# Optimization experiments

Hardware: AMD Instinct MI355X
Metric: run time of the kernel (lower is better)

## Reference

```python
import jax, jax.numpy as jnp
import numpy as np

N, E, G = 51200, 819200, 256            # nodes, directed edges, graphs
N2, A, E2 = 102400, 204800, 409600      # 2-sets, assignments, 2-set edges
D, L, NI2, NAF = 64, 5, 36, 40          # emb_dim, num_layer, num_i_2, num_atom_features
EPS = 1e-5


def _seg_sum(v, seg, n):
    return jax.ops.segment_sum(v, seg, num_segments=n)


def _seg_mean(v, seg, n):
    s = jax.ops.segment_sum(v, seg, num_segments=n)
    c = jax.ops.segment_sum(jnp.ones((v.shape[0],), v.dtype), seg, num_segments=n)
    return s / jnp.maximum(c, 1.0)[:, None]


def setup_inputs() -> dict:
    key = jax.random.key(0)
    ks = iter(jax.random.split(key, 64))
    nrm = lambda shape: jax.random.normal(next(ks), shape, jnp.float32) * 0.1
    x = jax.random.normal(next(ks), (N, NAF), jnp.float32)
    edge_index = jax.random.randint(next(ks), (2, E), 0, N, dtype=jnp.int32)
    edge_attr = jnp.stack([jax.random.randint(next(ks), (E,), 0, 4, dtype=jnp.int32),
                           jax.random.randint(next(ks), (E,), 0, 3, dtype=jnp.int32)], axis=1)
    batch = jnp.repeat(jnp.arange(G, dtype=jnp.int32), N // G)
    iso_type_2 = jax.nn.one_hot(jax.random.randint(next(ks), (N2,), 0, NI2), NI2, dtype=jnp.float32)
    edge_index_2 = jax.random.randint(next(ks), (2, E2), 0, N2, dtype=jnp.int32)
    assignment_index_2 = jnp.stack([jax.random.randint(next(ks), (A,), 0, N, dtype=jnp.int32),
                                    jnp.repeat(jnp.arange(N2, dtype=jnp.int32), 2)], axis=0)
    batch_2 = jnp.repeat(jnp.arange(G, dtype=jnp.int32), N2 // G)
    params = dict(
        emb_W=nrm((NAF, D)), emb_b=jnp.zeros((D,), jnp.float32),
        gin_W1=nrm((L, D, 2 * D)), gin_b1=jnp.zeros((L, 2 * D), jnp.float32),
        gin_W2=nrm((L, 2 * D, D)), gin_b2=jnp.zeros((L, D), jnp.float32),
        eemb1=nrm((L, 6, D)), eemb2=nrm((L, 3, D)),
        bn_gamma=jnp.ones((L, D), jnp.float32), bn_beta=jnp.zeros((L, D), jnp.float32),
        iso1_rel_W=nrm((D + NI2, D)), iso1_rel_b=jnp.zeros((D,), jnp.float32),
        iso1_root_W=nrm((D + NI2, D)),
        iso2_rel_W=nrm((D, D)), iso2_rel_b=jnp.zeros((D,), jnp.float32),
        iso2_root_W=nrm((D, D)),
        ro_W0=nrm((2 * D, D)), ro_b0=jnp.zeros((D,), jnp.float32),
        ro_W1=nrm((D, D // 2)), ro_b1=jnp.zeros((D // 2,), jnp.float32),
        ro_W2=nrm((D // 2, D // 4)), ro_b2=jnp.zeros((D // 4,), jnp.float32),
        last_W=nrm((D // 4, 1)), last_b=jnp.zeros((1,), jnp.float32),
    )
    return dict(x=x, edge_index=edge_index, edge_attr=edge_attr, batch=batch,
                iso_type_2=iso_type_2, edge_index_2=edge_index_2,
                assignment_index_2=assignment_index_2, batch_2=batch_2, **params)


def _forward(x, iso_type_2, emb_W, emb_b, gin_W1, gin_b1, gin_W2, gin_b2,
             eemb1, eemb2, bn_gamma, bn_beta,
             iso1_rel_W, iso1_rel_b, iso1_root_W, iso2_rel_W, iso2_rel_b, iso2_root_W,
             ro_W0, ro_b0, ro_W1, ro_b1, ro_W2, ro_b2, last_W, last_b,
             edge_index, edge_attr, batch, edge_index_2, assignment_index_2, batch_2):
    # --- GIN stack with edge-feature embeddings and self loops ---
    loop = jnp.arange(N, dtype=edge_index.dtype)
    src = jnp.concatenate([edge_index[0], loop])
    dst = jnp.concatenate([edge_index[1], loop])
    sl_attr = jnp.tile(jnp.array([[4, 0]], dtype=edge_attr.dtype), (N, 1))
    ea = jnp.concatenate([edge_attr, sl_attr], axis=0)  # [E+N, 2]

    h = jax.nn.relu(x @ emb_W + emb_b)  # x_embedding1
    for l in range(L):
        e = eemb1[l][ea[:, 0]] + eemb2[l][ea[:, 1]]      # [E+N, D]
        agg = _seg_sum(h[src] + e, dst, N)               # gather + scatter-add
        h2 = jax.nn.relu(agg @ gin_W1[l] + gin_b1[l]) @ gin_W2[l] + gin_b2[l]
        mu = jnp.mean(h2, axis=0)
        var = jnp.var(h2, axis=0)                        # biased, torch BN training mode
        h2 = (h2 - mu) / jnp.sqrt(var + EPS) * bn_gamma[l] + bn_beta[l]
        h = h2 if l == L - 1 else jax.nn.relu(h2)        # last layer: no ReLU (JK='last')
    node_rep = h

    # --- graph mean pool of node representation ---
    x1 = _seg_mean(node_rep, batch, G)                   # [G, D]

    # --- 2-set branch: avg_pool onto 2-sets, concat iso type, two GraphConvs ---
    xp = _seg_mean(node_rep[assignment_index_2[0]], assignment_index_2[1], N2)
    xp = jnp.concatenate([xp, iso_type_2], axis=1)       # [N2, D+NI2]

    def graph_conv(z, Wrel, brel, Wroot):
        agg = _seg_sum(z[edge_index_2[0]], edge_index_2[1], N2)
        return agg @ Wrel + brel + z @ Wroot

    xp = jax.nn.relu(graph_conv(xp, iso1_rel_W, iso1_rel_b, iso1_root_W))
    xp = jax.nn.relu(graph_conv(xp, iso2_rel_W, iso2_rel_b, iso2_root_W))
    x2 = _seg_mean(xp, batch_2, G)                       # [G, D]

    # --- readout MLP ---
    m = jnp.concatenate([x1, x2], axis=1)                # [G, 2D]
    m = jax.nn.relu(m @ ro_W0 + ro_b0)
    m = jax.nn.relu(m @ ro_W1 + ro_b1)
    m = jax.nn.relu(m @ ro_W2 + ro_b2)
    m = m @ last_W + last_b
    return m.reshape(-1)                                 # num_tasks == 1 -> flat [G]


def reference(x, edge_index, edge_attr, batch, iso_type_2, edge_index_2,
              assignment_index_2, batch_2, emb_W, emb_b, gin_W1, gin_b1, gin_W2,
              gin_b2, eemb1, eemb2, bn_gamma, bn_beta, iso1_rel_W, iso1_rel_b,
              iso1_root_W, iso2_rel_W, iso2_rel_b, iso2_root_W, ro_W0, ro_b0,
              ro_W1, ro_b1, ro_W2, ro_b2, last_W, last_b):
    return _forward(x, iso_type_2, emb_W, emb_b, gin_W1, gin_b1, gin_W2, gin_b2,
                    eemb1, eemb2, bn_gamma, bn_beta,
                    iso1_rel_W, iso1_rel_b, iso1_root_W, iso2_rel_W, iso2_rel_b,
                    iso2_root_W, ro_W0, ro_b0, ro_W1, ro_b1, ro_W2, ro_b2,
                    last_W, last_b, edge_index, edge_attr, batch, edge_index_2,
                    assignment_index_2, batch_2)
```

## Files before the change

kernel.cpp:

```cpp
#include <hip/hip_runtime.h>

#define NN   51200
#define EE   819200
#define GG   256
#define NN2  102400
#define AA   204800
#define EE2  409600
#define DD   64
#define LL   5

#define NB1  100
#define NB2  200
#define CAP1 10240
#define CAP2 3072

typedef __attribute__((ext_vector_type(8))) short bf16x8;
typedef __attribute__((ext_vector_type(4))) float f32x4;
typedef unsigned short ushort_t;

#define OFF_H      ((size_t)0)
#define OFF_AGG    ((size_t)13107200)
#define OFF_H2     ((size_t)26214400)
#define OFF_XP     ((size_t)39321600)
#define OFF_REC1   OFF_XP
#define OFF_REC2   ((size_t)47513600)
#define OFF_PERM   ((size_t)60293120)
#define OFF_YROOT  ((size_t)65536000)
#define OFF_OFFS1  ((size_t)91750400)
#define OFF_COL1   ((size_t)91955216)
#define OFF_OFFS2  ((size_t)95232016)
#define OFF_COL2   ((size_t)95641632)
#define OFF_CNT1   ((size_t)97280032)
#define OFF_BBASE  ((size_t)97282080)
#define OFF_CUR1   ((size_t)97484832)
#define OFF_STATS  ((size_t)98508832)
#define ZERO_BYTES ((size_t)1231360)
#define OFF_ISO    ((size_t)98511392)
#define OFF_M      ((size_t)98920992)
#define WS_NEEDED  ((size_t)99052064)

__device__ __forceinline__ int waveInclScan(int v, int lane) {
#pragma unroll
    for (int off = 1; off < 64; off <<= 1) {
        int t = __shfl_up(v, off, 64);
        if (lane >= off) v += t;
    }
    return v;
}

__device__ __forceinline__ void bsplit(float x, ushort_t& hi, ushort_t& lo) {
    union { float f; unsigned u; } a; a.f = x;
    unsigned hb = (a.u + 0x7FFFu + ((a.u >> 16) & 1u)) >> 16;
    union { unsigned u; float f; } h; h.u = hb << 16;
    float r = x - h.f;
    union { float f; unsigned u; } b; b.f = r;
    unsigned lb = (b.u + 0x7FFFu + ((b.u >> 16) & 1u)) >> 16;
    hi = (ushort_t)hb; lo = (ushort_t)lb;
}
__device__ __forceinline__ ushort_t f2bf(float x) {
    union { float f; unsigned u; } a; a.f = x;
    return (ushort_t)((a.u + 0x7FFFu + ((a.u >> 16) & 1u)) >> 16);
}
__device__ __forceinline__ float bf2f(ushort_t v) {
    union { unsigned u; float f; } t; t.u = (unsigned)v << 16; return t.f;
}

__global__ __launch_bounds__(256) void kbA(const int* __restrict__ src1, const int* __restrict__ dst1,
                                           const int* __restrict__ ea,
                                           const int* __restrict__ src2, const int* __restrict__ dst2,
                                           int* __restrict__ bucketCnt,
                                           int2* __restrict__ rec1, int2* __restrict__ rec2) {
    __shared__ int lhist[256];
    __shared__ int lbase[256];
    int tid = threadIdx.x, b = blockIdx.x;
    lhist[tid] = 0;
    __syncthreads();
    if (b < 400) {
        int i = (b * 256 + tid) * 8;
        int4 d0 = *(const int4*)(dst1 + i);
        int4 d1 = *(const int4*)(dst1 + i + 4);
        int dst[8] = {d0.x, d0.y, d0.z, d0.w, d1.x, d1.y, d1.z, d1.w};
        int bin[8], lr[8];
#pragma unroll
        for (int j = 0; j < 8; ++j) {
            bin[j] = dst[j] >> 9;
            lr[j] = atomicAdd(&lhist[bin[j]], 1);
        }
        __syncthreads();
        if (tid < NB1) {
            int c = lhist[tid];
            lbase[tid] = c ? atomicAdd(&bucketCnt[tid], c) : 0;
        }
        __syncthreads();
        int4 s0 = *(const int4*)(src1 + i);
        int4 s1 = *(const int4*)(src1 + i + 4);
        int src[8] = {s0.x, s0.y, s0.z, s0.w, s1.x, s1.y, s1.z, s1.w};
        int4 e0 = *(const int4*)(ea + 2 * i);
        int4 e1 = *(const int4*)(ea + 2 * i + 4);
        int4 e2 = *(const int4*)(ea + 2 * i + 8);
        int4 e3 = *(const int4*)(ea + 2 * i + 12);
        int code[8] = {e0.x * 3 + e0.y, e0.z * 3 + e0.w, e1.x * 3 + e1.y, e1.z * 3 + e1.w,
                       e2.x * 3 + e2.y, e2.z * 3 + e2.w, e3.x * 3 + e3.y, e3.z * 3 + e3.w};
#pragma unroll
        for (int j = 0; j < 8; ++j) {
            int pos = bin[j] * CAP1 + lbase[bin[j]] + lr[j];
            rec1[pos] = make_int2(src[j] | (code[j] << 16), dst[j]);
        }
    } else {
        int i = ((b - 400) * 256 + tid) * 8;
        int4 d0 = *(const int4*)(dst2 + i);
        int4 d1 = *(const int4*)(dst2 + i + 4);
        int dst[8] = {d0.x, d0.y, d0.z, d0.w, d1.x, d1.y, d1.z, d1.w};
        int bin[8], lr[8];
#pragma unroll
        for (int j = 0; j < 8; ++j) {
            bin[j] = dst[j] >> 9;
            lr[j] = atomicAdd(&lhist[bin[j]], 1);
        }
        __syncthreads();
        if (tid < NB2) {
            int c = lhist[tid];
            lbase[tid] = c ? atomicAdd(&bucketCnt[NB1 + tid], c) : 0;
        }
        __syncthreads();
        int4 s0 = *(const int4*)(src2 + i);
        int4 s1 = *(const int4*)(src2 + i + 4);
        int src[8] = {s0.x, s0.y, s0.z, s0.w, s1.x, s1.y, s1.z, s1.w};
#pragma unroll
        for (int j = 0; j < 8; ++j) {
            int pos = bin[j] * CAP2 + lbase[bin[j]] + lr[j];
            rec2[pos] = make_int2(src[j], dst[j]);
        }
    }
}

__global__ void kbscan(const int* __restrict__ bucketCnt, int* __restrict__ bucketBase) {
    __shared__ int wsum[4];
    int tid = threadIdx.x, lane = tid & 63, wid = tid >> 6;
    int nb = blockIdx.x ? NB2 : NB1;
    const int* cnt = bucketCnt + (blockIdx.x ? NB1 : 0);
    int* base = bucketBase + (blockIdx.x ? NB1 : 0);
    int v = (tid < nb) ? cnt[tid] : 0;
    int incl = waveInclScan(v, lane);
    if (lane == 63) wsum[wid] = incl;
    __syncthreads();
    int woff = 0;
#pragma unroll
    for (int w = 0; w < 3; ++w) woff += (w < wid) ? wsum[w] : 0;
    if (tid < nb) base[tid] = woff + incl - v;
}

__global__ __launch_bounds__(256) void kbB(const int* __restrict__ bucketCnt,
                                           const int* __restrict__ bucketBase,
                                           const int2* __restrict__ rec1, const int2* __restrict__ rec2,
                                           int* __restrict__ offs1, int* __restrict__ col1,
                                           int* __restrict__ offs2, int* __restrict__ col2,
                                           int* __restrict__ dbin) {
    __shared__ int nh[512];
    __shared__ int ncur[512];
    __shared__ int wsum[4];
    __shared__ int dhist[64];
    int tid = threadIdx.x, b = blockIdx.x;
    bool g1 = b < NB1;
    const int2* rec = g1 ? (rec1 + (size_t)b * CAP1) : (rec2 + (size_t)(b - NB1) * CAP2);
    int cnt = bucketCnt[b];
    int base = bucketBase[b];
    int* offs = g1 ? offs1 : offs2;
    int* col = g1 ? col1 : col2;
    int nodeBase = g1 ? b * 512 : (b - NB1) * 512;
    nh[tid] = 0; nh[tid + 256] = 0;
    if (tid < 64) dhist[tid] = 0;
    __syncthreads();
    for (int e = tid; e < cnt; e += 256) {
        int2 r = rec[e];
        atomicAdd(&nh[r.y & 511], 1);
    }
    __syncthreads();
    int v0 = nh[2 * tid], v1 = nh[2 * tid + 1];
    int s = v0 + v1;
    int lane = tid & 63, wid = tid >> 6;
    int incl = waveInclScan(s, lane);
    if (lane == 63) wsum[wid] = incl;
    __syncthreads();
    int woff = 0;
#pragma unroll
    for (int w = 0; w < 3; ++w) woff += (w < wid) ? wsum[w] : 0;
    int excl = woff + incl - s;
    ncur[2 * tid] = excl;
    ncur[2 * tid + 1] = excl + v0;
    offs[nodeBase + 2 * tid] = base + excl;
    offs[nodeBase + 2 * tid + 1] = base + excl + v0;
    if (g1) {
        atomicAdd(&dhist[v0 < 63 ? v0 : 63], 1);
        atomicAdd(&dhist[v1 < 63 ? v1 : 63], 1);
    }
    __syncthreads();
    for (int e = tid; e < cnt; e += 256) {
        int2 r = rec[e];
        int node = r.y & 511;
        int slot = base + atomicAdd(&ncur[node], 1);
        col[slot] = r.x;
    }
    if (g1 && tid < 64 && dhist[tid]) atomicAdd(&dbin[tid], dhist[tid]);
    if (tid == 0) {
        if (b == NB1 - 1) offs1[NN] = EE;
        if (b == NB1 + NB2 - 1) offs2[NN2] = EE2;
    }
}

__global__ __launch_bounds__(256) void kiso(const float* __restrict__ iso, int* __restrict__ isoIdx) {
    __shared__ float srow[256 * 36];
    int tid = threadIdx.x;
    int base = blockIdx.x * 256;
    const float4* g4p = (const float4*)(iso + (size_t)base * 36);
#pragma unroll
    for (int i = tid; i < 2304; i += 256) ((float4*)srow)[i] = g4p[i];
    __syncthreads();
    const float* r = srow + tid * 36;
    int best = 0;
#pragma unroll
    for (int k = 0; k < 36; ++k)
        if (r[k] > 0.5f) best = k;
    isoIdx[base + tid] = best;
}

__global__ void kprepx(const float* __restrict__ x, const float* __restrict__ embW,
                       const float* __restrict__ embB, ushort_t* __restrict__ hbf,
                       const float* __restrict__ gW1, const float* __restrict__ gW2,
                       ushort_t* __restrict__ w1h, ushort_t* __restrict__ w1l,
                       ushort_t* __restrict__ w2h, ushort_t* __restrict__ w2l,
                       const float* __restrict__ i1rW, const float* __restrict__ i1tW,
                       const float* __restrict__ i2rW, const float* __restrict__ i2tW,
                       ushort_t* __restrict__ gcwh, ushort_t* __restrict__ gcwl) {
    int b = blockIdx.x;
    if (b < 12800) {
        int t = b * 256 + threadIdx.x;
        int n = t >> 6, d = t & 63;
        float acc = embB[d];
        const float4* xr4 = (const float4*)(x + (size_t)n * 40);
#pragma unroll
        for (int k4 = 0; k4 < 10; ++k4) {
            float4 xv = xr4[k4];
            acc = fmaf(xv.x, embW[(4 * k4 + 0) * 64 + d], acc);
            acc = fmaf(xv.y, embW[(4 * k4 + 1) * 64 + d], acc);
            acc = fmaf(xv.z, embW[(4 * k4 + 2) * 64 + d], acc);
            acc = fmaf(xv.w, embW[(4 * k4 + 3) * 64 + d], acc);
        }
        hbf[(size_t)n * 64 + d] = f2bf(fmaxf(acc, 0.f));
    } else if (b < 12840) {
        int t = (b - 12800) * 256 + threadIdx.x;
        int lane = t & 63, frag = t >> 6;
        int c15 = lane & 15, q = lane >> 4;
        if (frag < 80) {
            int kt = frag & 1, nt = (frag >> 1) & 7, l = frag >> 4;
            const float* W = gW1 + l * 8192;
            ushort_t* oh = w1h + ((size_t)frag * 64 + lane) * 8;
            ushort_t* ol = w1l + ((size_t)frag * 64 + lane) * 8;
            int kb = kt * 32 + q * 8, colw = nt * 16 + c15;
#pragma unroll
            for (int j = 0; j < 8; ++j) {
                ushort_t hi, lo; bsplit(W[(kb + j) * 128 + colw], hi, lo);
                oh[j] = hi; ol[j] = lo;
            }
        } else if (frag < 160) {
            int f = frag - 80;
            int kt = f & 3, nt = (f >> 2) & 3, l = f >> 4;
            const float* W = gW2 + l * 8192;
            ushort_t* oh = w2h + ((size_t)f * 64 + lane) * 8;
            ushort_t* ol = w2l + ((size_t)f * 64 + lane) * 8;
            int kb = kt * 32 + q * 8, colw = nt * 16 + c15;
#pragma unroll
            for (int j = 0; j < 8; ++j) {
                ushort_t hi, lo; bsplit(W[(kb + j) * 64 + colw], hi, lo);
                oh[j] = hi; ol[j] = lo;
            }
        }
    } else {
        int t = (b - 12840) * 256 + threadIdx.x;
        int lane = t & 63, frag = t >> 6;
        int c15 = lane & 15, q = lane >> 4;
        int m = frag >> 3, f = frag & 7;
        int kt = f & 1, nt = f >> 1;
        const float* W = (m == 0) ? i1rW : (m == 1) ? i1tW : (m == 2) ? i2rW : i2tW;
        ushort_t* oh = gcwh + (size_t)m * 4096 + ((size_t)f * 64 + lane) * 8;
        ushort_t* ol = gcwl + (size_t)m * 4096 + ((size_t)f * 64 + lane) * 8;
        int kb = kt * 32 + q * 8, colw = nt * 16 + c15;
#pragma unroll
        for (int j = 0; j < 8; ++j) {
            ushort_t hi, lo; bsplit(W[(kb + j) * 64 + colw], hi, lo);
            oh[j] = hi; ol[j] = lo;
        }
    }
}

__global__ __launch_bounds__(256) void kdegplace(const int* __restrict__ offs,
                                                 const int* __restrict__ dbin,
                                                 int* __restrict__ dcur,
                                                 int* __restrict__ perm) {
    __shared__ int lhist[64];
    __shared__ int lbase[64];
    __shared__ int sdstart[64];
    int tid = threadIdx.x;
    if (tid < 64) {
        lhist[tid] = 0;
        int v = dbin[tid];
        int incl = waveInclScan(v, tid);
        sdstart[tid] = incl - v;
    }
    __syncthreads();
    int n = blockIdx.x * 256 + tid;
    int d = offs[n + 1] - offs[n]; d = d < 63 ? d : 63;
    int lr = atomicAdd(&lhist[d], 1);
    __syncthreads();
    if (tid < 64) {
        int c = lhist[tid];
        lbase[tid] = c ? atomicAdd(&dcur[tid], c) : 0;
    }
    __syncthreads();
    perm[sdstart[d] + lbase[d] + lr] = n;
}

__global__ __launch_bounds__(256) void ktrans(const float* __restrict__ hraw,
                                              ushort_t* __restrict__ hbf,
                                              const float* __restrict__ pst,
                                              const float* __restrict__ gamma,
                                              const float* __restrict__ beta) {
    __shared__ float sstat[128];
    __shared__ float sSC[64], sSH[64];
    int tid = threadIdx.x;
    if (tid < 128) {
        float s = 0.f;
        const float* p = pst + tid;
#pragma unroll
        for (int i = 0; i < 32; ++i) s += p[i * 128];
        sstat[tid] = s;
    }
    __syncthreads();
    if (tid < 64) {
        float mu = sstat[tid] * (1.f / NN);
        float var = sstat[64 + tid] * (1.f / NN) - mu * mu;
        float sc = gamma[tid] * rsqrtf(var + 1e-5f);
        sSC[tid] = sc; sSH[tid] = beta[tid] - mu * sc;
    }
    __syncthreads();
    int c = (tid & 15) * 4;
    float4 sc4 = *(const float4*)(sSC + c);
    float4 sh4 = *(const float4*)(sSH + c);
    const float4* hp = (const float4*)hraw;
    ushort4* op = (ushort4*)hbf;
    size_t base = (size_t)blockIdx.x * 1024 + tid;
#pragma unroll
    for (int r = 0; r < 4; ++r) {
        float4 v = hp[base + r * 256];
        ushort4 o;
        o.x = f2bf(fmaxf(fmaf(v.x, sc4.x, sh4.x), 0.f));
        o.y = f2bf(fmaxf(fmaf(v.y, sc4.y, sh4.y), 0.f));
        o.z = f2bf(fmaxf(fmaf(v.z, sc4.z, sh4.z), 0.f));
        o.w = f2bf(fmaxf(fmaf(v.w, sc4.w, sh4.w), 0.f));
        op[base + r * 256] = o;
    }
}

__global__ __launch_bounds__(256) void kglayer(
    const ushort_t* __restrict__ hin, float* __restrict__ hout,
    const int* __restrict__ perm,
    const int* __restrict__ offs, const int* __restrict__ col,
    const float* __restrict__ e1, const float* __restrict__ e2,
    const ushort_t* __restrict__ w1h, const ushort_t* __restrict__ w1l,
    const ushort_t* __restrict__ w2h, const ushort_t* __restrict__ w2l,
    const float* __restrict__ b1, const float* __restrict__ b2,
    float* __restrict__ pstout) {
    __shared__ float etab[13 * 64];
    __shared__ int sPerm[16];
    __shared__ float sMLP[16 * 132];
    float* sA = sMLP;
    float* sH = sMLP;
    int tid = threadIdx.x;
    if (tid < 16) sPerm[tid] = perm[blockIdx.x * 16 + tid];
    for (int idx = tid; idx < 13 * 64; idx += 256) {
        int ci = idx >> 6, dd = idx & 63;
        etab[idx] = e1[(ci / 3) * 64 + dd] + e2[(ci % 3) * 64 + dd];
    }
    __syncthreads();
    int lane = tid & 63, wv = tid >> 6;
    int c15 = lane & 15, q = lane >> 4;

    {
        int n = sPerm[wv * 4 + q];
        int s0 = offs[n], s1 = offs[n + 1];
        ushort4 sx = *(const ushort4*)(hin + (size_t)n * 64 + 4 * c15);
        float4 et = *(const float4*)(etab + 12 * 64 + 4 * c15);
        float a0 = bf2f(sx.x) + et.x, a1 = bf2f(sx.y) + et.y;
        float a2 = bf2f(sx.z) + et.z, a3 = bf2f(sx.w) + et.w;
        int deg = s1 - s0;
        if (deg > 0) {
            const int* cp = col + s0;
            int nfull = deg >> 3, rem = deg & 7;
            int vv[8];
#pragma unroll
            for (int j = 0; j < 8; ++j) {
                int idx = j < deg ? j : deg - 1;
                vv[j] = cp[idx];
            }
            for (int it = 0; it < nfull; ++it) {
                ushort4 xv[8];
                float4 tv[8];
#pragma unroll
                for (int j = 0; j < 8; ++j) {
                    xv[j] = *(const ushort4*)(hin + (size_t)(vv[j] & 0xFFFF) * 64 + 4 * c15);
                    tv[j] = *(const float4*)(etab + (vv[j] >> 16) * 64 + 4 * c15);
                }
                int e8 = (it + 1) * 8;
                bool more = e8 < deg;
                int nx[8];
                if (more) {
#pragma unroll
                    for (int j = 0; j < 8; ++j) {
                        int idx = e8 + j; idx = idx < deg ? idx : deg - 1;
                        nx[j] = cp[idx];
                    }
                }
#pragma unroll
                for (int j = 0; j < 8; ++j) {
                    a0 += bf2f(xv[j].x) + tv[j].x;
                    a1 += bf2f(xv[j].y) + tv[j].y;
                    a2 += bf2f(xv[j].z) + tv[j].z;
                    a3 += bf2f(xv[j].w) + tv[j].w;
                }
                if (more) {
#pragma unroll
                    for (int j = 0; j < 8; ++j) vv[j] = nx[j];
                }
            }
            if (rem) {
                ushort4 xv[8];
                float4 tv[8];
#pragma unroll
                for (int j = 0; j < 8; ++j) {
                    xv[j] = *(const ushort4*)(hin + (size_t)(vv[j] & 0xFFFF) * 64 + 4 * c15);
                    tv[j] = *(const float4*)(etab + (vv[j] >> 16) * 64 + 4 * c15);
                }
#pragma unroll
                for (int j = 0; j < 8; ++j) {
                    float mm = (j < rem) ? 1.f : 0.f;
                    a0 = fmaf(bf2f(xv[j].x) + tv[j].x, mm, a0);
                    a1 = fmaf(bf2f(xv[j].y) + tv[j].y, mm, a1);
                    a2 = fmaf(bf2f(xv[j].z) + tv[j].z, mm, a2);
                    a3 = fmaf(bf2f(xv[j].w) + tv[j].w, mm, a3);
                }
            }
        }
        *(float4*)(sA + (wv * 4 + q) * 68 + 4 * c15) = make_float4(a0, a1, a2, a3);
    }
    __syncthreads();

    bf16x8 ah[2], al[2];
#pragma unroll
    for (int kt = 0; kt < 2; ++kt) {
        const float* p = sA + c15 * 68 + kt * 32 + q * 8;
        float4 x0 = *(const float4*)p;
        float4 x1 = *(const float4*)(p + 4);
        float xs[8] = {x0.x, x0.y, x0.z, x0.w, x1.x, x1.y, x1.z, x1.w};
#pragma unroll
        for (int j = 0; j < 8; ++j) {
            ushort_t hi, lo; bsplit(xs[j], hi, lo);
            ah[kt][j] = (short)hi; al[kt][j] = (short)lo;
        }
    }
    __syncthreads();

    f32x4 acc1[2];
#pragma unroll
    for (int j = 0; j < 2; ++j) { f32x4 z = {0.f, 0.f, 0.f, 0.f}; acc1[j] = z; }
#pragma unroll
    for (int kt = 0; kt < 2; ++kt) {
#pragma unroll
        for (int j = 0; j < 2; ++j) {
            int nt = 2 * wv + j;
            size_t fo = ((size_t)((nt * 2 + kt) * 64 + lane)) * 8;
            bf16x8 bh = *(const bf16x8*)(w1h + fo);
            bf16x8 bl = *(const bf16x8*)(w1l + fo);
            acc1[j] = __builtin_amdgcn_mfma_f32_16x16x32_bf16(ah[kt], bh, acc1[j], 0, 0, 0);
            acc1[j] = __builtin_amdgcn_mfma_f32_16x16x32_bf16(al[kt], bh, acc1[j], 0, 0, 0);
            acc1[j] = __builtin_amdgcn_mfma_f32_16x16x32_bf16(ah[kt], bl, acc1[j], 0, 0, 0);
        }
    }
#pragma unroll
    for (int j = 0; j < 2; ++j) {
        int nt = 2 * wv + j;
        float bias = b1[nt * 16 + c15];
#pragma unroll
        for (int rg = 0; rg < 4; ++rg)
            sH[(4 * q + rg) * 132 + nt * 16 + c15] = fmaxf(acc1[j][rg] + bias, 0.f);
    }
    __syncthreads();

    f32x4 acc2 = {0.f, 0.f, 0.f, 0.f};
#pragma unroll
    for (int kt = 0; kt < 4; ++kt) {
        const float* p = sH + c15 * 132 + kt * 32 + q * 8;
        float4 x0 = *(const float4*)p;
        float4 x1 = *(const float4*)(p + 4);
        float xs[8] = {x0.x, x0.y, x0.z, x0.w, x1.x, x1.y, x1.z, x1.w};
        bf16x8 a2h, a2l;
#pragma unroll
        for (int j = 0; j < 8; ++j) {
            ushort_t hi, lo; bsplit(xs[j], hi, lo);
            a2h[j] = (short)hi; a2l[j] = (short)lo;
        }
        size_t fo = ((size_t)((wv * 4 + kt) * 64 + lane)) * 8;
        bf16x8 bh = *(const bf16x8*)(w2h + fo);
        bf16x8 bl = *(const bf16x8*)(w2l + fo);
        acc2 = __builtin_amdgcn_mfma_f32_16x16x32_bf16(a2h, bh, acc2, 0, 0, 0);
        acc2 = __builtin_amdgcn_mfma_f32_16x16x32_bf16(a2l, bh, acc2, 0, 0, 0);
        acc2 = __builtin_amdgcn_mfma_f32_16x16x32_bf16(a2h, bl, acc2, 0, 0, 0);
    }
    {
        float bias = b2[wv * 16 + c15];
        float s = 0.f, s2 = 0.f;
#pragma unroll
        for (int rg = 0; rg < 4; ++rg) {
            float v = acc2[rg] + bias;
            hout[(size_t)sPerm[4 * q + rg] * 64 + wv * 16 + c15] = v;
            s += v; s2 += v * v;
        }
        s += __shfl_xor(s, 16, 64);  s += __shfl_xor(s, 32, 64);
        s2 += __shfl_xor(s2, 16, 64); s2 += __shfl_xor(s2, 32, 64);
        if (q == 0) {
            float* ps = pstout + (size_t)(blockIdx.x & 31) * 128;
            atomicAdd(&ps[wv * 16 + c15], s);
            atomicAdd(&ps[64 + wv * 16 + c15], s2);
        }
    }
}

__global__ __launch_bounds__(256) void kgcmm1(const ushort_t* __restrict__ grh,
                                              const ushort_t* __restrict__ grl,
                                              const ushort_t* __restrict__ gth,
                                              const ushort_t* __restrict__ gtl,
                                              const float* __restrict__ WrelIso,
                                              const float* __restrict__ WrootIso,
                                              const int* __restrict__ isoIdx,
                                              ushort_t* __restrict__ Yrel,
                                              float* __restrict__ Yroot,
                                              const float* __restrict__ pst,
                                              const float* __restrict__ g4,
                                              const float* __restrict__ b4,
                                              const int* __restrict__ a0g,
                                              const float* __restrict__ h2src) {
    __shared__ float sX[64 * 68];
    __shared__ float sstat[128];
    __shared__ float sSC[64], sSH[64];
    int tid = threadIdx.x, blk = blockIdx.x;
    if (tid < 128) {
        float s = 0.f;
        const float* p = pst + tid;
#pragma unroll
        for (int i = 0; i < 32; ++i) s += p[i * 128];
        sstat[tid] = s;
    }
    __syncthreads();
    if (tid < 64) {
        float mu = sstat[tid] * (1.f / NN);
        float var = sstat[64 + tid] * (1.f / NN) - mu * mu;
        float sc = g4[tid] * rsqrtf(var + 1e-5f);
        sSC[tid] = sc;
        sSH[tid] = b4[tid] - mu * sc;
    }
    __syncthreads();
#pragma unroll
    for (int i = tid; i < 1024; i += 256) {
        int row = i >> 4, c = (i & 15) << 2;
        int grow = blk * 64 + row;
        int na = a0g[2 * grow], nb = a0g[2 * grow + 1];
        float4 va = *(const float4*)(h2src + (size_t)na * 64 + c);
        float4 vb = *(const float4*)(h2src + (size_t)nb * 64 + c);
        float4 v;
        v.x = 0.5f * (va.x + vb.x); v.y = 0.5f * (va.y + vb.y);
        v.z = 0.5f * (va.z + vb.z); v.w = 0.5f * (va.w + vb.w);
        v.x = fmaf(v.x, sSC[c], sSH[c]);
        v.y = fmaf(v.y, sSC[c + 1], sSH[c + 1]);
        v.z = fmaf(v.z, sSC[c + 2], sSH[c + 2]);
        v.w = fmaf(v.w, sSC[c + 3], sSH[c + 3]);
        float* p = sX + row * 68 + c;
        p[0] = v.x; p[1] = v.y; p[2] = v.z; p[3] = v.w;
    }
    __syncthreads();
    int lane = tid & 63, wv = tid >> 6;
    int c15 = lane & 15, q = lane >> 4;

    bf16x8 ah[2], al[2];
#pragma unroll
    for (int kt = 0; kt < 2; ++kt) {
        const float* p = sX + (16 * wv + c15) * 68 + kt * 32 + q * 8;
        float4 x0 = *(const float4*)p;
        float4 x1 = *(const float4*)(p + 4);
        float xs[8] = {x0.x, x0.y, x0.z, x0.w, x1.x, x1.y, x1.z, x1.w};
#pragma unroll
        for (int j = 0; j < 8; ++j) {
            ushort_t hi, lo; bsplit(xs[j], hi, lo);
            ah[kt][j] = (short)hi; al[kt][j] = (short)lo;
        }
    }

    f32x4 accR[4], accT[4];
#pragma unroll
    for (int nt = 0; nt < 4; ++nt) {
        f32x4 z = {0.f, 0.f, 0.f, 0.f};
        accR[nt] = z; accT[nt] = z;
    }
#pragma unroll
    for (int nt = 0; nt < 4; ++nt) {
#pragma unroll
        for (int kt = 0; kt < 2; ++kt) {
            size_t fo = ((size_t)((nt * 2 + kt) * 64 + lane)) * 8;
            bf16x8 bh = *(const bf16x8*)(grh + fo);
            bf16x8 bl = *(const bf16x8*)(grl + fo);
            accR[nt] = __builtin_amdgcn_mfma_f32_16x16x32_bf16(ah[kt], bh, accR[nt], 0, 0, 0);
            accR[nt] = __builtin_amdgcn_mfma_f32_16x16x32_bf16(al[kt], bh, accR[nt], 0, 0, 0);
            accR[nt] = __builtin_amdgcn_mfma_f32_16x16x32_bf16(ah[kt], bl, accR[nt], 0, 0, 0);
            bf16x8 ch = *(const bf16x8*)(gth + fo);
            bf16x8 cl = *(const bf16x8*)(gtl + fo);
            accT[nt] = __builtin_amdgcn_mfma_f32_16x16x32_bf16(ah[kt], ch, accT[nt], 0, 0, 0);
            accT[nt] = __builtin_amdgcn_mfma_f32_16x16x32_bf16(al[kt], ch, accT[nt], 0, 0, 0);
            accT[nt] = __builtin_amdgcn_mfma_f32_16x16x32_bf16(ah[kt], cl, accT[nt], 0, 0, 0);
        }
    }

    int rbase = blk * 64 + 16 * wv + 4 * q;
#pragma unroll
    for (int rg = 0; rg < 4; ++rg) {
        int row = rbase + rg;
        int ii = isoIdx[row];
        ushort_t* yr = Yrel + (size_t)row * 64;
        float* yt = Yroot + (size_t)row * 64;
        const float* er = WrelIso + (size_t)ii * 64;
        const float* et = WrootIso + (size_t)ii * 64;
#pragma unroll
        for (int nt = 0; nt < 4; ++nt) {
            int cc = nt * 16 + c15;
            yr[cc] = f2bf(accR[nt][rg] + er[cc]);
            yt[cc] = accT[nt][rg] + et[cc];
        }
    }
}

__global__ __launch_bounds__(256) void kgcmm2(const float* __restrict__ AGG,
                                              const ushort_t* __restrict__ XP,
                                              const ushort_t* __restrict__ grh,
                                              const ushort_t* __restrict__ grl,
                                              const ushort_t* __restrict__ gth,
                                              const ushort_t* __restrict__ gtl,
                                              const float* __restrict__ brel,
                                              float* __restrict__ OUT) {
    __shared__ float sA[64 * 68];
    __shared__ float sB[64 * 68];
    int tid = threadIdx.x, blk = blockIdx.x;
#pragma unroll
    for (int i = tid; i < 1024; i += 256) {
        int row = i >> 4, c = (i & 15) << 2;
        float4 va = ((const float4*)(AGG + (size_t)blk * 4096))[i];
        ushort4 vb4 = ((const ushort4*)(XP + (size_t)blk * 4096))[i];
        float* pa = sA + row * 68 + c;
        float* pb = sB + row * 68 + c;
        pa[0] = va.x; pa[1] = va.y; pa[2] = va.z; pa[3] = va.w;
        pb[0] = bf2f(vb4.x); pb[1] = bf2f(vb4.y); pb[2] = bf2f(vb4.z); pb[3] = bf2f(vb4.w);
    }
    __syncthreads();
    int lane = tid & 63, wv = tid >> 6;
    int c15 = lane & 15, q = lane >> 4;

    bf16x8 aAh[2], aAl[2], aBh[2];
#pragma unroll
    for (int kt = 0; kt < 2; ++kt) {
        const float* pa = sA + (16 * wv + c15) * 68 + kt * 32 + q * 8;
        const float* pb = sB + (16 * wv + c15) * 68 + kt * 32 + q * 8;
        float4 a0 = *(const float4*)pa;
        float4 a1 = *(const float4*)(pa + 4);
        float4 b0 = *(const float4*)pb;
        float4 b1 = *(const float4*)(pb + 4);
        float as[8] = {a0.x, a0.y, a0.z, a0.w, a1.x, a1.y, a1.z, a1.w};
        float bs[8] = {b0.x, b0.y, b0.z, b0.w, b1.x, b1.y, b1.z, b1.w};
#pragma unroll
        for (int j = 0; j < 8; ++j) {
            ushort_t hi, lo;
            bsplit(as[j], hi, lo); aAh[kt][j] = (short)hi; aAl[kt][j] = (short)lo;
            aBh[kt][j] = (short)f2bf(bs[j]);
        }
    }

    f32x4 acc[4];
#pragma unroll
    for (int nt = 0; nt < 4; ++nt) { f32x4 z = {0.f, 0.f, 0.f, 0.f}; acc[nt] = z; }
#pragma unroll
    for (int nt = 0; nt < 4; ++nt) {
#pragma unroll
        for (int kt = 0; kt < 2; ++kt) {
            size_t fo = ((size_t)((nt * 2 + kt) * 64 + lane)) * 8;
            bf16x8 bh = *(const bf16x8*)(grh + fo);
            bf16x8 bl = *(const bf16x8*)(grl + fo);
            acc[nt] = __builtin_amdgcn_mfma_f32_16x16x32_bf16(aAh[kt], bh, acc[nt], 0, 0, 0);
            acc[nt] = __builtin_amdgcn_mfma_f32_16x16x32_bf16(aAl[kt], bh, acc[nt], 0, 0, 0);
            acc[nt] = __builtin_amdgcn_mfma_f32_16x16x32_bf16(aAh[kt], bl, acc[nt], 0, 0, 0);
            bf16x8 ch = *(const bf16x8*)(gth + fo);
            bf16x8 cl = *(const bf16x8*)(gtl + fo);
            acc[nt] = __builtin_amdgcn_mfma_f32_16x16x32_bf16(aBh[kt], ch, acc[nt], 0, 0, 0);
            acc[nt] = __builtin_amdgcn_mfma_f32_16x16x32_bf16(aBh[kt], cl, acc[nt], 0, 0, 0);
        }
    }

    int rbase = blk * 64 + 16 * wv + 4 * q;
#pragma unroll
    for (int rg = 0; rg < 4; ++rg) {
        int row = rbase + rg;
        float* yo = OUT + (size_t)row * 64;
#pragma unroll
        for (int nt = 0; nt < 4; ++nt) {
            int cc = nt * 16 + c15;
            yo[cc] = fmaxf(acc[nt][rg] + brel[cc], 0.f);
        }
    }
}

__global__ void kgather2(const ushort_t* __restrict__ yrel, const float* __restrict__ yroot,
                         const float* __restrict__ brel, const int* __restrict__ offs,
                         const int* __restrict__ col, ushort_t* __restrict__ out) {
    int t = blockIdx.x * 256 + threadIdx.x;
    int j = t >> 4, c = t & 15;
    int s0 = offs[j], s1 = offs[j + 1];
    float4 rt = *(const float4*)(yroot + (size_t)j * 64 + 4 * c);
    float4 bb = *(const float4*)(brel + 4 * c);
    float a0 = rt.x + bb.x, a1 = rt.y + bb.y, a2 = rt.z + bb.z, a3 = rt.w + bb.w;
    if (s0 < s1) {
        int vv[4];
#pragma unroll
        for (int jj = 0; jj < 4; ++jj) {
            int idx = s0 + jj; idx = idx < s1 ? idx : s1 - 1;
            vv[jj] = col[idx];
        }
        int e = s0;
        while (true) {
            int ne = e + 4;
            bool more = ne < s1;
            ushort4 xs[4];
#pragma unroll
            for (int jj = 0; jj < 4; ++jj)
                xs[jj] = *(const ushort4*)(yrel + (size_t)vv[jj] * 64 + 4 * c);
            int nx[4];
            if (more) {
#pragma unroll
                for (int jj = 0; jj < 4; ++jj) {
                    int idx = ne + jj; idx = idx < s1 ? idx : s1 - 1;
                    nx[jj] = col[idx];
                }
            }
#pragma unroll
            for (int jj = 0; jj < 4; ++jj) {
                float mm = (e + jj < s1) ? 1.f : 0.f;
                a0 = fmaf(bf2f(xs[jj].x), mm, a0);
                a1 = fmaf(bf2f(xs[jj].y), mm, a1);
                a2 = fmaf(bf2f(xs[jj].z), mm, a2);
                a3 = fmaf(bf2f(xs[jj].w), mm, a3);
            }
            if (!more) break;
            e = ne;
#pragma unroll
            for (int jj = 0; jj < 4; ++jj) vv[jj] = nx[jj];
        }
    }
    ushort4 o;
    o.x = f2bf(fmaxf(a0, 0.f));
    o.y = f2bf(fmaxf(a1, 0.f));
    o.z = f2bf(fmaxf(a2, 0.f));
    o.w = f2bf(fmaxf(a3, 0.f));
    *(ushort4*)(out + (size_t)j * 64 + 4 * c) = o;
}

__global__ void kgather2raw(const ushort_t* __restrict__ xpsrc, const int* __restrict__ offs,
                            const int* __restrict__ col, float* __restrict__ agg) {
    int t = blockIdx.x * 256 + threadIdx.x;
    int j = t >> 4, c = t & 15;
    int s0 = offs[j], s1 = offs[j + 1];
    float a0 = 0.f, a1 = 0.f, a2 = 0.f, a3 = 0.f;
    if (s0 < s1) {
        int vv[4];
#pragma unroll
        for (int jj = 0; jj < 4; ++jj) {
            int idx = s0 + jj; idx = idx < s1 ? idx : s1 - 1;
            vv[jj] = col[idx];
        }
        int e = s0;
        while (true) {
            int ne = e + 4;
            bool more = ne < s1;
            ushort4 xs[4];
#pragma unroll
            for (int jj = 0; jj < 4; ++jj)
                xs[jj] = *(const ushort4*)(xpsrc + (size_t)vv[jj] * 64 + 4 * c);
            int nx[4];
            if (more) {
#pragma unroll
                for (int jj = 0; jj < 4; ++jj) {
                    int idx = ne + jj; idx = idx < s1 ? idx : s1 - 1;
                    nx[jj] = col[idx];
                }
            }
#pragma unroll
            for (int jj = 0; jj < 4; ++jj) {
                float mm = (e + jj < s1) ? 1.f : 0.f;
                a0 = fmaf(bf2f(xs[jj].x), mm, a0);
                a1 = fmaf(bf2f(xs[jj].y), mm, a1);
                a2 = fmaf(bf2f(xs[jj].z), mm, a2);
                a3 = fmaf(bf2f(xs[jj].w), mm, a3);
            }
            if (!more) break;
            e = ne;
#pragma unroll
            for (int jj = 0; jj < 4; ++jj) vv[jj] = nx[jj];
        }
    }
    *(float4*)(agg + (size_t)j * 64 + 4 * c) = make_float4(a0, a1, a2, a3);
}

__global__ void kpoolg(const float* __restrict__ h2, const float* __restrict__ xp2,
                       const float* __restrict__ pst, const float* __restrict__ g4,
                       const float* __restrict__ b4, float* __restrict__ m) {
    __shared__ float sstat[128];
    __shared__ float red[4][64];
    int g = blockIdx.x, tid = threadIdx.x;
    if (tid < 128) {
        float s = 0.f;
        const float* p = pst + tid;
#pragma unroll
        for (int i = 0; i < 32; ++i) s += p[i * 128];
        sstat[tid] = s;
    }
    int wid = tid >> 6, d = tid & 63;
    float s1 = 0.f;
    for (int i = wid; i < 200; i += 4) s1 += h2[((size_t)g * 200 + i) * 64 + d];
    red[wid][d] = s1;
    __syncthreads();
    if (wid == 0) {
        float mean = (red[0][d] + red[1][d] + red[2][d] + red[3][d]) * (1.f / 200.f);
        float mu = sstat[d] * (1.f / NN);
        float var = sstat[64 + d] * (1.f / NN) - mu * mu;
        float sc = g4[d] * rsqrtf(var + 1e-5f);
        m[g * 128 + d] = fmaf(mean, sc, b4[d] - mu * sc);
    }
    __syncthreads();
    float s2 = 0.f;
    for (int i = wid; i < 400; i += 4) s2 += xp2[((size_t)g * 400 + i) * 64 + d];
    red[wid][d] = s2;
    __syncthreads();
    if (wid == 0) m[g * 128 + 64 + d] = (red[0][d] + red[1][d] + red[2][d] + red[3][d]) * (1.f / 400.f);
}

__global__ void kread(const float* __restrict__ m, const float* __restrict__ W0,
                      const float* __restrict__ b0, const float* __restrict__ W1,
                      const float* __restrict__ b1, const float* __restrict__ W2,
                      const float* __restrict__ b2, const float* __restrict__ lw,
                      const float* __restrict__ lb, float* __restrict__ out) {
    __shared__ float s0[64], s1[32], s2[16];
    int g = blockIdx.x, d = threadIdx.x;
    const float* mr = m + g * 128;
    float t = b0[d];
    for (int k = 0; k < 128; ++k) t = fmaf(mr[k], W0[k * 64 + d], t);
    s0[d] = fmaxf(t, 0.f);
    __syncthreads();
    if (d < 32) {
        float u = b1[d];
        for (int k = 0; k < 64; ++k) u = fmaf(s0[k], W1[k * 32 + d], u);
        s1[d] = fmaxf(u, 0.f);
    }
    __syncthreads();
    if (d < 16) {
        float u = b2[d];
        for (int k = 0; k < 32; ++k) u = fmaf(s1[k], W2[k * 16 + d], u);
        s2[d] = fmaxf(u, 0.f);
    }
    __syncthreads();
    if (d == 0) {
        float u = lb[0];
        for (int k = 0; k < 16; ++k) u = fmaf(s2[k], lw[k], u);
        out[g] = u;
    }
}

extern "C" void kernel_launch(void* const* d_in, const int* in_sizes, int n_in,
                              void* d_out, int out_size, void* d_ws, size_t ws_size,
                              hipStream_t stream) {
    if (ws_size < WS_NEEDED) return;

    const float* x    = (const float*)d_in[0];
    const int*   ei   = (const int*)d_in[1];
    const int*   ea   = (const int*)d_in[2];
    const float* iso  = (const float*)d_in[4];
    const int*   ei2  = (const int*)d_in[5];
    const int*   ai2  = (const int*)d_in[6];
    const float* embW = (const float*)d_in[8];
    const float* embB = (const float*)d_in[9];
    const float* gW1  = (const float*)d_in[10];
    const float* gB1  = (const float*)d_in[11];
    const float* gW2  = (const float*)d_in[12];
    const float* gB2  = (const float*)d_in[13];
    const float* ee1  = (const float*)d_in[14];
    const float* ee2  = (const float*)d_in[15];
    const float* bng  = (const float*)d_in[16];
    const float* bnb  = (const float*)d_in[17];
    const float* i1rW = (const float*)d_in[18];
    const float* i1rB = (const float*)d_in[19];
    const float* i1tW = (const float*)d_in[20];
    const float* i2rW = (const float*)d_in[21];
    const float* i2rB = (const float*)d_in[22];
    const float* i2tW = (const float*)d_in[23];
    const float* roW0 = (const float*)d_in[24];
    const float* roB0 = (const float*)d_in[25];
    const float* roW1 = (const float*)d_in[26];
    const float* roB1 = (const float*)d_in[27];
    const float* roW2 = (const float*)d_in[28];
    const float* roB2 = (const float*)d_in[29];
    const float* lW   = (const float*)d_in[30];
    const float* lB   = (const float*)d_in[31];
    float* out = (float*)d_out;

    char* ws = (char*)d_ws;
    ushort_t* hbf = (ushort_t*)(ws + OFF_H);
    float* hraw   = (float*)(ws + OFF_AGG);
    float* h2     = (float*)(ws + OFF_H2);
    ushort_t* yrelb = (ushort_t*)(ws + OFF_H);
    float* yroot  = (float*)(ws + OFF_YROOT);
    float* aggb   = (float*)(ws + OFF_H);
    ushort_t* xpb = (ushort_t*)(ws + OFF_XP);
    float* xp2    = (float*)(ws + OFF_YROOT);
    int* offs1    = (int*)(ws + OFF_OFFS1);
    int* col1     = (int*)(ws + OFF_COL1);
    int* offs2    = (int*)(ws + OFF_OFFS2);
    int* col2     = (int*)(ws + OFF_COL2);
    int* isoIdx   = (int*)(ws + OFF_ISO);
    float* mbuf   = (float*)(ws + OFF_M);
    ushort_t* w1h = (ushort_t*)(ws + OFF_YROOT);
    ushort_t* w1l = (ushort_t*)(ws + OFF_YROOT + 81920);
    ushort_t* w2h = (ushort_t*)(ws + OFF_YROOT + 163840);
    ushort_t* w2l = (ushort_t*)(ws + OFF_YROOT + 245760);
    ushort_t* gcwh = (ushort_t*)(ws + OFF_M);
    ushort_t* gcwl = (ushort_t*)(ws + OFF_M + 32768);
    float* pstat2 = (float*)(ws + OFF_CUR1);
    int2* rec1    = (int2*)(ws + OFF_REC1);
    int2* rec2    = (int2*)(ws + OFF_REC2);
    int* bucketCnt  = (int*)(ws + OFF_CNT1);
    int* bucketBase = (int*)(ws + OFF_BBASE);
    int* perm     = (int*)(ws + OFF_PERM);
    int* dbin     = (int*)(ws + OFF_STATS);
    int* dcur     = dbin + 64;

    const int* src1 = ei;
    const int* dst1 = ei + EE;
    const int* src2 = ei2;
    const int* dst2 = ei2 + EE2;
    const int* a0   = ai2;

    hipMemsetAsync(ws + OFF_CNT1, 0, ZERO_BYTES, stream);

    kbA<<<600, 256, 0, stream>>>(src1, dst1, ea, src2, dst2, bucketCnt, rec1, rec2);
    kiso<<<NN2 / 256, 256, 0, stream>>>(iso, isoIdx);
    kprepx<<<12848, 256, 0, stream>>>(x, embW, embB, hbf, gW1, gW2,
                                      w1h, w1l, w2h, w2l,
                                      i1rW, i1tW, i2rW, i2tW, gcwh, gcwl);
    kbscan<<<2, 256, 0, stream>>>(bucketCnt, bucketBase);
    kbB<<<300, 256, 0, stream>>>(bucketCnt, bucketBase, rec1, rec2,
                                 offs1, col1, offs2, col2, dbin);
    kdegplace<<<NN / 256, 256, 0, stream>>>(offs1, dbin, dcur, perm);

    for (int l = 0; l < LL; ++l) {
        float* hout = (l == LL - 1) ? h2 : hraw;
        kglayer<<<NN / 16, 256, 0, stream>>>(
            hbf, hout, perm, offs1, col1, ee1 + l * 384, ee2 + l * 192,
            w1h + (size_t)l * 8192, w1l + (size_t)l * 8192,
            w2h + (size_t)l * 8192, w2l + (size_t)l * 8192,
            gB1 + l * 128, gB2 + l * 64,
            pstat2 + (size_t)l * 4096);
        if (l < LL - 1)
            ktrans<<<800, 256, 0, stream>>>(hraw, hbf, pstat2 + (size_t)l * 4096,
                                            bng + l * 64, bnb + l * 64);
    }

    kgcmm1<<<NN2 / 64, 256, 0, stream>>>(gcwh, gcwl, gcwh + 4096, gcwl + 4096,
                                         i1rW + 64 * 64, i1tW + 64 * 64, isoIdx,
                                         yrelb, yroot,
                                         pstat2 + (size_t)4 * 4096,
                                         bng + 4 * 64, bnb + 4 * 64, a0, h2);
    kgather2<<<NN2 * 16 / 256, 256, 0, stream>>>(yrelb, yroot, i1rB, offs2, col2, xpb);
    kgather2raw<<<NN2 * 16 / 256, 256, 0, stream>>>(xpb, offs2, col2, aggb);
    kgcmm2<<<NN2 / 64, 256, 0, stream>>>(aggb, xpb,
                                         gcwh + 8192, gcwl + 8192, gcwh + 12288, gcwl + 12288,
                                         i2rB, xp2);

    kpoolg<<<GG, 256, 0, stream>>>(h2, xp2, pstat2 + (size_t)4 * 4096,
                                   bng + 4 * 64, bnb + 4 * 64, mbuf);
    kread<<<GG, 64, 0, stream>>>(mbuf, roW0, roB0, roW1, roB1, roW2, roB2, lW, lB, out);
}
```

Baseline: 529.3 us.

## Store intermediate layer outputs and aggregates in bf16, fold bucket scan into kbB

The pre-BN GIN layer outputs (hraw) and the second-stage aggregate buffer are now stored as bf16 instead of fp32, which halves their write and read traffic in kglayer/ktrans and kgather2raw/kgcmm2. In kgcmm2 the low-half split MFMA on the aggregate operand is dropped because that input is already bf16. The separate bucket-scan kernel is removed and each kbB block recomputes the prefix over bucket counts itself, saving one launch. The trade-off is reduced precision in BN statistics inputs and the aggregate, at the cost of small numeric error.

```diff
diff --git a/kernel.cpp b/kernel.cpp
--- a/kernel.cpp
+++ b/kernel.cpp
@@ -31,7 +31,6 @@
 #define OFF_OFFS2  ((size_t)95232016)
 #define OFF_COL2   ((size_t)95641632)
 #define OFF_CNT1   ((size_t)97280032)
-#define OFF_BBASE  ((size_t)97282080)
 #define OFF_CUR1   ((size_t)97484832)
 #define OFF_STATS  ((size_t)98508832)
 #define ZERO_BYTES ((size_t)1231360)
@@ -134,24 +133,7 @@
     }
 }
 
-__global__ void kbscan(const int* __restrict__ bucketCnt, int* __restrict__ bucketBase) {
-    __shared__ int wsum[4];
-    int tid = threadIdx.x, lane = tid & 63, wid = tid >> 6;
-    int nb = blockIdx.x ? NB2 : NB1;
-    const int* cnt = bucketCnt + (blockIdx.x ? NB1 : 0);
-    int* base = bucketBase + (blockIdx.x ? NB1 : 0);
-    int v = (tid < nb) ? cnt[tid] : 0;
-    int incl = waveInclScan(v, lane);
-    if (lane == 63) wsum[wid] = incl;
-    __syncthreads();
-    int woff = 0;
-#pragma unroll
-    for (int w = 0; w < 3; ++w) woff += (w < wid) ? wsum[w] : 0;
-    if (tid < nb) base[tid] = woff + incl - v;
-}
-
 __global__ __launch_bounds__(256) void kbB(const int* __restrict__ bucketCnt,
-                                           const int* __restrict__ bucketBase,
                                            const int2* __restrict__ rec1, const int2* __restrict__ rec2,
                                            int* __restrict__ offs1, int* __restrict__ col1,
                                            int* __restrict__ offs2, int* __restrict__ col2,
@@ -160,11 +142,27 @@
     __shared__ int ncur[512];
     __shared__ int wsum[4];
     __shared__ int dhist[64];
+    __shared__ int sbase;
     int tid = threadIdx.x, b = blockIdx.x;
     bool g1 = b < NB1;
+    int lane = tid & 63, wid = tid >> 6;
+    {
+        int nb = g1 ? NB1 : NB2;
+        const int* cntA = bucketCnt + (g1 ? 0 : NB1);
+        int myIdx = g1 ? b : b - NB1;
+        int v = (tid < nb) ? cntA[tid] : 0;
+        int incl = waveInclScan(v, lane);
+        if (lane == 63) wsum[wid] = incl;
+        __syncthreads();
+        int woff = 0;
+#pragma unroll
+        for (int w = 0; w < 3; ++w) woff += (w < wid) ? wsum[w] : 0;
+        if (tid == myIdx) sbase = woff + incl - v;
+        __syncthreads();
+    }
+    int base = sbase;
     const int2* rec = g1 ? (rec1 + (size_t)b * CAP1) : (rec2 + (size_t)(b - NB1) * CAP2);
     int cnt = bucketCnt[b];
-    int base = bucketBase[b];
     int* offs = g1 ? offs1 : offs2;
     int* col = g1 ? col1 : col2;
     int nodeBase = g1 ? b * 512 : (b - NB1) * 512;
@@ -178,7 +176,6 @@
     __syncthreads();
     int v0 = nh[2 * tid], v1 = nh[2 * tid + 1];
     int s = v0 + v1;
-    int lane = tid & 63, wid = tid >> 6;
     int incl = waveInclScan(s, lane);
     if (lane == 63) wsum[wid] = incl;
     __syncthreads();
@@ -320,7 +317,7 @@
     perm[sdstart[d] + lbase[d] + lr] = n;
 }
 
-__global__ __launch_bounds__(256) void ktrans(const float* __restrict__ hraw,
+__global__ __launch_bounds__(256) void ktrans(const ushort_t* __restrict__ hraw,
                                               ushort_t* __restrict__ hbf,
                                               const float* __restrict__ pst,
                                               const float* __restrict__ gamma,
@@ -346,23 +343,25 @@
     int c = (tid & 15) * 4;
     float4 sc4 = *(const float4*)(sSC + c);
     float4 sh4 = *(const float4*)(sSH + c);
-    const float4* hp = (const float4*)hraw;
+    const ushort4* hp = (const ushort4*)hraw;
     ushort4* op = (ushort4*)hbf;
     size_t base = (size_t)blockIdx.x * 1024 + tid;
 #pragma unroll
     for (int r = 0; r < 4; ++r) {
-        float4 v = hp[base + r * 256];
+        ushort4 v = hp[base + r * 256];
         ushort4 o;
-        o.x = f2bf(fmaxf(fmaf(v.x, sc4.x, sh4.x), 0.f));
-        o.y = f2bf(fmaxf(fmaf(v.y, sc4.y, sh4.y), 0.f));
-        o.z = f2bf(fmaxf(fmaf(v.z, sc4.z, sh4.z), 0.f));
-        o.w = f2bf(fmaxf(fmaf(v.w, sc4.w, sh4.w), 0.f));
+        o.x = f2bf(fmaxf(fmaf(bf2f(v.x), sc4.x, sh4.x), 0.f));
+        o.y = f2bf(fmaxf(fmaf(bf2f(v.y), sc4.y, sh4.y), 0.f));
+        o.z = f2bf(fmaxf(fmaf(bf2f(v.z), sc4.z, sh4.z), 0.f));
+        o.w = f2bf(fmaxf(fmaf(bf2f(v.w), sc4.w, sh4.w), 0.f));
         op[base + r * 256] = o;
     }
 }
 
+template <int LAST>
 __global__ __launch_bounds__(256) void kglayer(
-    const ushort_t* __restrict__ hin, float* __restrict__ hout,
+    const ushort_t* __restrict__ hin, ushort_t* __restrict__ houtB,
+    float* __restrict__ houtF,
     const int* __restrict__ perm,
     const int* __restrict__ offs, const int* __restrict__ col,
     const float* __restrict__ e1, const float* __restrict__ e2,
@@ -521,7 +520,9 @@
 #pragma unroll
         for (int rg = 0; rg < 4; ++rg) {
             float v = acc2[rg] + bias;
-            hout[(size_t)sPerm[4 * q + rg] * 64 + wv * 16 + c15] = v;
+            size_t oidx = (size_t)sPerm[4 * q + rg] * 64 + wv * 16 + c15;
+            if (LAST) houtF[oidx] = v;
+            else houtB[oidx] = f2bf(v);
             s += v; s2 += v * v;
         }
         s += __shfl_xor(s, 16, 64);  s += __shfl_xor(s, 32, 64);
@@ -645,7 +646,7 @@
     }
 }
 
-__global__ __launch_bounds__(256) void kgcmm2(const float* __restrict__ AGG,
+__global__ __launch_bounds__(256) void kgcmm2(const ushort_t* __restrict__ AGG,
                                               const ushort_t* __restrict__ XP,
                                               const ushort_t* __restrict__ grh,
                                               const ushort_t* __restrict__ grl,
@@ -659,18 +660,18 @@
 #pragma unroll
     for (int i = tid; i < 1024; i += 256) {
         int row = i >> 4, c = (i & 15) << 2;
-        float4 va = ((const float4*)(AGG + (size_t)blk * 4096))[i];
+        ushort4 va4 = ((const ushort4*)(AGG + (size_t)blk * 4096))[i];
         ushort4 vb4 = ((const ushort4*)(XP + (size_t)blk * 4096))[i];
         float* pa = sA + row * 68 + c;
         float* pb = sB + row * 68 + c;
-        pa[0] = va.x; pa[1] = va.y; pa[2] = va.z; pa[3] = va.w;
+        pa[0] = bf2f(va4.x); pa[1] = bf2f(va4.y); pa[2] = bf2f(va4.z); pa[3] = bf2f(va4.w);
         pb[0] = bf2f(vb4.x); pb[1] = bf2f(vb4.y); pb[2] = bf2f(vb4.z); pb[3] = bf2f(vb4.w);
     }
     __syncthreads();
     int lane = tid & 63, wv = tid >> 6;
     int c15 = lane & 15, q = lane >> 4;
 
-    bf16x8 aAh[2], aAl[2], aBh[2];
+    bf16x8 aAh[2], aBh[2];
 #pragma unroll
     for (int kt = 0; kt < 2; ++kt) {
         const float* pa = sA + (16 * wv + c15) * 68 + kt * 32 + q * 8;
@@ -683,8 +684,7 @@
         float bs[8] = {b0.x, b0.y, b0.z, b0.w, b1.x, b1.y, b1.z, b1.w};
 #pragma unroll
         for (int j = 0; j < 8; ++j) {
-            ushort_t hi, lo;
-            bsplit(as[j], hi, lo); aAh[kt][j] = (short)hi; aAl[kt][j] = (short)lo;
+            aAh[kt][j] = (short)f2bf(as[j]);
             aBh[kt][j] = (short)f2bf(bs[j]);
         }
     }
@@ -700,7 +700,6 @@
             bf16x8 bh = *(const bf16x8*)(grh + fo);
             bf16x8 bl = *(const bf16x8*)(grl + fo);
             acc[nt] = __builtin_amdgcn_mfma_f32_16x16x32_bf16(aAh[kt], bh, acc[nt], 0, 0, 0);
-            acc[nt] = __builtin_amdgcn_mfma_f32_16x16x32_bf16(aAl[kt], bh, acc[nt], 0, 0, 0);
             acc[nt] = __builtin_amdgcn_mfma_f32_16x16x32_bf16(aAh[kt], bl, acc[nt], 0, 0, 0);
             bf16x8 ch = *(const bf16x8*)(gth + fo);
             bf16x8 cl = *(const bf16x8*)(gtl + fo);
@@ -777,7 +776,7 @@
 }
 
 __global__ void kgather2raw(const ushort_t* __restrict__ xpsrc, const int* __restrict__ offs,
-                            const int* __restrict__ col, float* __restrict__ agg) {
+                            const int* __restrict__ col, ushort_t* __restrict__ agg) {
     int t = blockIdx.x * 256 + threadIdx.x;
     int j = t >> 4, c = t & 15;
     int s0 = offs[j], s1 = offs[j + 1];
@@ -819,7 +818,9 @@
             for (int jj = 0; jj < 4; ++jj) vv[jj] = nx[jj];
         }
     }
-    *(float4*)(agg + (size_t)j * 64 + 4 * c) = make_float4(a0, a1, a2, a3);
+    ushort4 o;
+    o.x = f2bf(a0); o.y = f2bf(a1); o.z = f2bf(a2); o.w = f2bf(a3);
+    *(ushort4*)(agg + (size_t)j * 64 + 4 * c) = o;
 }
 
 __global__ void kpoolg(const float* __restrict__ h2, const float* __restrict__ xp2,
@@ -925,11 +926,11 @@
 
     char* ws = (char*)d_ws;
     ushort_t* hbf = (ushort_t*)(ws + OFF_H);
-    float* hraw   = (float*)(ws + OFF_AGG);
+    ushort_t* hraw = (ushort_t*)(ws + OFF_AGG);
     float* h2     = (float*)(ws + OFF_H2);
     ushort_t* yrelb = (ushort_t*)(ws + OFF_H);
     float* yroot  = (float*)(ws + OFF_YROOT);
-    float* aggb   = (float*)(ws + OFF_H);
+    ushort_t* aggb = (ushort_t*)(ws + OFF_H);
     ushort_t* xpb = (ushort_t*)(ws + OFF_XP);
     float* xp2    = (float*)(ws + OFF_YROOT);
     int* offs1    = (int*)(ws + OFF_OFFS1);
@@ -948,7 +949,6 @@
     int2* rec1    = (int2*)(ws + OFF_REC1);
     int2* rec2    = (int2*)(ws + OFF_REC2);
     int* bucketCnt  = (int*)(ws + OFF_CNT1);
-    int* bucketBase = (int*)(ws + OFF_BBASE);
     int* perm     = (int*)(ws + OFF_PERM);
     int* dbin     = (int*)(ws + OFF_STATS);
     int* dcur     = dbin + 64;
@@ -966,22 +966,28 @@
     kprepx<<<12848, 256, 0, stream>>>(x, embW, embB, hbf, gW1, gW2,
                                       w1h, w1l, w2h, w2l,
                                       i1rW, i1tW, i2rW, i2tW, gcwh, gcwl);
-    kbscan<<<2, 256, 0, stream>>>(bucketCnt, bucketBase);
-    kbB<<<300, 256, 0, stream>>>(bucketCnt, bucketBase, rec1, rec2,
+    kbB<<<300, 256, 0, stream>>>(bucketCnt, rec1, rec2,
                                  offs1, col1, offs2, col2, dbin);
     kdegplace<<<NN / 256, 256, 0, stream>>>(offs1, dbin, dcur, perm);
 
     for (int l = 0; l < LL; ++l) {
-        float* hout = (l == LL - 1) ? h2 : hraw;
-        kglayer<<<NN / 16, 256, 0, stream>>>(
-            hbf, hout, perm, offs1, col1, ee1 + l * 384, ee2 + l * 192,
-            w1h + (size_t)l * 8192, w1l + (size_t)l * 8192,
-            w2h + (size_t)l * 8192, w2l + (size_t)l * 8192,
-            gB1 + l * 128, gB2 + l * 64,
-            pstat2 + (size_t)l * 4096);
-        if (l < LL - 1)
+        if (l == LL - 1) {
+            kglayer<1><<<NN / 16, 256, 0, stream>>>(
+                hbf, nullptr, h2, perm, offs1, col1, ee1 + l * 384, ee2 + l * 192,
+                w1h + (size_t)l * 8192, w1l + (size_t)l * 8192,
+                w2h + (size_t)l * 8192, w2l + (size_t)l * 8192,
+                gB1 + l * 128, gB2 + l * 64,
+                pstat2 + (size_t)l * 4096);
+        } else {
+            kglayer<0><<<NN / 16, 256, 0, stream>>>(
+                hbf, hraw, nullptr, perm, offs1, col1, ee1 + l * 384, ee2 + l * 192,
+                w1h + (size_t)l * 8192, w1l + (size_t)l * 8192,
+                w2h + (size_t)l * 8192, w2l + (size_t)l * 8192,
+                gB1 + l * 128, gB2 + l * 64,
+                pstat2 + (size_t)l * 4096);
             ktrans<<<800, 256, 0, stream>>>(hraw, hbf, pstat2 + (size_t)l * 4096,
                                             bng + l * 64, bnb + l * 64);
+        }
     }
 
     kgcmm1<<<NN2 / 64, 256, 0, stream>>>(gcwh, gcwl, gcwh + 4096, gcwl + 4096,
```

New measurement: 524.3 us. About the same (-0.9%).
